# Kernel tuning notes

Hardware: AMD Instinct MI355X
Metric: run time of the kernel (lower is better)

Reference implementation:

```python
import jax, jax.numpy as jnp
import numpy as np

B, T, F, H = 64, 256, 64, 64


def setup_inputs() -> dict:
    key = jax.random.key(0)
    k = jax.random.split(key, 20)
    X_f = jax.random.normal(k[0], (B, T, F), jnp.float32)
    M_f = (jax.random.uniform(k[1], (B, T, F)) < 0.8).astype(jnp.float32)
    D_f = jax.random.uniform(k[2], (B, T, F), jnp.float32)
    # backward stream = time-reversed data with its own deltas (as in PyPOTS pipeline)
    X_b = jnp.flip(X_f, axis=1)
    M_b = jnp.flip(M_f, axis=1)
    D_b = jax.random.uniform(k[3], (B, T, F), jnp.float32)
    s = 1.0 / np.sqrt(H).astype(np.float32)
    def u(kk, shape):
        return jax.random.uniform(kk, shape, jnp.float32, minval=-s, maxval=s)
    params = dict(
        w_ih_f=u(k[4], (3 * H, 3)), w_hh_f=u(k[5], (3 * H, H)),
        b_ih_f=u(k[6], (3 * H,)), b_hh_f=u(k[7], (3 * H,)),
        w_ih_b=u(k[8], (3 * H, 3)), w_hh_b=u(k[9], (3 * H, H)),
        b_ih_b=u(k[10], (3 * H,)), b_hh_b=u(k[11], (3 * H,)),
        W_proj=u(k[12], (1, 2 * H)), b_proj=u(k[13], (1,)),
        U=u(k[14], (F, F)), V1=u(k[15], (F, F)), V2=u(k[16], (F, F)),
        beta=u(k[17], (F,)), W_fin=u(k[18], (F, F)), b_fin=u(k[19], (F,)),
    )
    return dict(X_f=X_f, M_f=M_f, D_f=D_f, X_b=X_b, M_b=M_b, D_b=D_b, **params)


def _gru_scan(xs, w_ih, w_hh, b_ih, b_hh):
    # xs: [T, N, 3] -> hidden states [T, N, H]; torch GRUCell math
    N = xs.shape[1]
    h0 = jnp.zeros((N, H), xs.dtype)
    def step(h, x):
        gi = x @ w_ih.T + b_ih          # [N, 3H]
        gh = h @ w_hh.T + b_hh          # [N, 3H]
        i_r, i_z, i_n = jnp.split(gi, 3, axis=-1)
        h_r, h_z, h_n = jnp.split(gh, 3, axis=-1)
        r = jax.nn.sigmoid(i_r + h_r)
        z = jax.nn.sigmoid(i_z + h_z)
        n = jnp.tanh(i_n + r * h_n)
        h_new = (1.0 - z) * n + z * h
        return h_new, h_new
    _, hs = jax.lax.scan(step, h0, xs)
    return hs


def _calc_rmse(pred, target, mask):
    se = jnp.sum(((pred - target) * mask) ** 2)
    return jnp.sqrt(se / (jnp.sum(mask) + 1e-12))


def reference(X_f, M_f, D_f, X_b, M_b, D_b,
              w_ih_f, w_hh_f, b_ih_f, b_hh_f,
              w_ih_b, w_hh_b, b_ih_b, b_hh_b,
              W_proj, b_proj, U, V1, V2, beta, W_fin, b_fin):
    # Fold the per-feature loop into the batch axis: N = B*F, shared GRU weights.
    def pack(X, M, D):
        inp = jnp.stack([X, M, D], axis=-1)          # [B, T, F, 3]
        return inp.transpose(1, 0, 2, 3).reshape(T, B * F, 3)
    hs_f = _gru_scan(pack(X_f, M_f, D_f), w_ih_f, w_hh_f, b_ih_f, b_hh_f)  # [T, BF, H]
    hs_b = _gru_scan(pack(X_b, M_b, D_b), w_ih_b, w_hh_b, b_ih_b, b_hh_b)
    hs_b = jnp.flip(hs_b, axis=0)
    cat = jnp.concatenate([hs_f, hs_b], axis=-1)     # [T, BF, 2H]
    est = cat @ W_proj.T + b_proj                    # [T, BF, 1]
    RNN_estimation = est.reshape(T, B, F).transpose(1, 0, 2)  # [B, T, F]
    X, M = X_f, M_f
    RNN_imputed = M * X + (1.0 - M) * RNN_estimation
    m = 1.0 - jnp.eye(F, dtype=X.dtype)
    h = jnp.tanh(X @ (U * m).T + RNN_imputed @ (V1 * m).T + M @ V2.T + beta)
    FCN_estimation = h @ W_fin.T + b_fin
    imputed_data = M * X + (1.0 - M) * FCN_estimation
    loss = _calc_rmse(FCN_estimation, X, M) + _calc_rmse(RNN_estimation, X, M)
    return imputed_data, loss
```

## Files before the change

kernel.cpp:

```cpp
#include <hip/hip_runtime.h>
#include <math.h>

#define B_ 64
#define T_ 256
#define F_ 64
#define H_ 64
#define NROW (B_ * F_)

typedef short bf16x8 __attribute__((ext_vector_type(8)));
typedef float f32x4  __attribute__((ext_vector_type(4)));

__device__ __forceinline__ float rcp_f(float x) {
  float r; asm("v_rcp_f32 %0, %1" : "=v"(r) : "v"(x)); return r;
}
__device__ __forceinline__ float sigm(float x) {
  return rcp_f(1.0f + __expf(-x));
}
__device__ __forceinline__ float tanh_f(float y) {
  return fmaf(-2.0f, rcp_f(1.0f + __expf(2.0f * y)), 1.0f);
}
__device__ __forceinline__ unsigned short bf16_rne(float v) {
  unsigned u = __float_as_uint(v);
  unsigned r = u + 0x7FFFu + ((u >> 16) & 1u);
  return (unsigned short)(r >> 16);
}

#define MFMA16(a, b, c) __builtin_amdgcn_mfma_f32_16x16x32_bf16((a), (b), (c), 0, 0, 0)

__global__ void __launch_bounds__(256, 2)
gru_kernel(const float* __restrict__ Xf, const float* __restrict__ Mf, const float* __restrict__ Df,
           const float* __restrict__ Xb, const float* __restrict__ Mb, const float* __restrict__ Db,
           const float* __restrict__ wih_f, const float* __restrict__ whh_f,
           const float* __restrict__ bih_f, const float* __restrict__ bhh_f,
           const float* __restrict__ wih_b, const float* __restrict__ whh_b,
           const float* __restrict__ bih_b, const float* __restrict__ bhh_b,
           const float* __restrict__ Wproj,
           float* __restrict__ est_f, float* __restrict__ est_b)
{
  __shared__ float          s_xmd[256][3][16];
  __shared__ unsigned short s_h[2][16][72];

  const int tid  = threadIdx.x;
  const int lane = tid & 63;
  const int wid  = tid >> 6;
  const int dir  = blockIdx.x >> 8;
  const int n0   = (blockIdx.x & 255) * 16;
  const int b0   = n0 >> 6;
  const int f0   = n0 & 63;

  const float* X   = dir ? Xb    : Xf;
  const float* M   = dir ? Mb    : Mf;
  const float* D   = dir ? Db    : Df;
  const float* wih = dir ? wih_b : wih_f;
  const float* whh = dir ? whh_b : whh_f;
  const float* bih = dir ? bih_b : bih_f;
  const float* bhh = dir ? bhh_b : bhh_f;
  float* est       = dir ? est_b : est_f;

  const int u     = 16 * wid + (lane & 15);
  const int ucol  = u;
  const int g8    = (lane >> 4) * 8;
  const int arow  = lane & 15;
  const int rbase = (lane >> 4) * 4;

  bf16x8 Bhi[3][2], Blo[3][2];
#pragma unroll
  for (int gt = 0; gt < 3; ++gt) {
#pragma unroll
    for (int kh = 0; kh < 2; ++kh) {
      const float* wp = &whh[(gt * 64 + u) * 64 + kh * 32 + g8];
#pragma unroll
      for (int j = 0; j < 8; ++j) {
        float v = wp[j];
        unsigned short hb = bf16_rne(v);
        float fhi = __uint_as_float((unsigned)hb << 16);
        Bhi[gt][kh][j] = (short)hb;
        Blo[gt][kh][j] = (short)bf16_rne(v - fhi);
      }
    }
  }

  bf16x8 Bp_hi0, Bp_hi1, Bp_lo0, Bp_lo1;
#pragma unroll
  for (int j = 0; j < 8; ++j) {
    float v0 = ((lane & 15) == 0) ? Wproj[dir * 64 + 0 * 32 + g8 + j] : 0.0f;
    float v1 = ((lane & 15) == 0) ? Wproj[dir * 64 + 1 * 32 + g8 + j] : 0.0f;
    unsigned short h0 = bf16_rne(v0), h1 = bf16_rne(v1);
    float f0h = __uint_as_float((unsigned)h0 << 16);
    float f1h = __uint_as_float((unsigned)h1 << 16);
    Bp_hi0[j] = (short)h0; Bp_hi1[j] = (short)h1;
    Bp_lo0[j] = (short)bf16_rne(v0 - f0h);
    Bp_lo1[j] = (short)bf16_rne(v1 - f1h);
  }

  const float wir0 = wih[(0 * 64 + u) * 3 + 0], wir1 = wih[(0 * 64 + u) * 3 + 1], wir2 = wih[(0 * 64 + u) * 3 + 2];
  const float wiz0 = wih[(1 * 64 + u) * 3 + 0], wiz1 = wih[(1 * 64 + u) * 3 + 1], wiz2 = wih[(1 * 64 + u) * 3 + 2];
  const float win0 = wih[(2 * 64 + u) * 3 + 0], win1 = wih[(2 * 64 + u) * 3 + 1], win2 = wih[(2 * 64 + u) * 3 + 2];
  const float br  = bih[0 * 64 + u] + bhh[0 * 64 + u];
  const float bz  = bih[1 * 64 + u] + bhh[1 * 64 + u];
  const float bin = bih[2 * 64 + u];
  const float bhn = bhh[2 * 64 + u];

  {
    const int f  = tid & 15;
    const int t0 = tid >> 4;
    const size_t rowbase = (size_t)b0 * 256 * 64 + f0 + f;
#pragma unroll 1
    for (int c = 0; c < 16; ++c) {
      int t = t0 + 16 * c;
      size_t gidx = rowbase + (size_t)t * 64;
      s_xmd[t][0][f] = X[gidx];
      s_xmd[t][1][f] = M[gidx];
      s_xmd[t][2][f] = D[gidx];
    }
  }
  for (int i = tid; i < 2 * 16 * 72; i += 256)
    ((unsigned short*)s_h)[i] = 0;
  __syncthreads();

  f32x4 hold = {0.f, 0.f, 0.f, 0.f};

#pragma unroll 2
  for (int t = 0; t < 256; ++t) {
    const int cur = t & 1, nxt = cur ^ 1;

    bf16x8 Ahi0 = *(const bf16x8*)&s_h[cur][arow][g8];
    bf16x8 Ahi1 = *(const bf16x8*)&s_h[cur][arow][32 + g8];

    if (t > 0 && wid == ((t - 1) & 3)) {
      f32x4 Cp = {0.f, 0.f, 0.f, 0.f};
      Cp = MFMA16(Ahi0, Bp_hi0, Cp); Cp = MFMA16(Ahi1, Bp_hi1, Cp);
      Cp = MFMA16(Ahi0, Bp_lo0, Cp); Cp = MFMA16(Ahi1, Bp_lo1, Cp);
      if ((lane & 15) == 0) {
        int tp = t - 1;
        int tt = dir ? (255 - tp) : tp;
        *(f32x4*)&est[(size_t)tt * NROW + n0 + rbase] = Cp;
      }
    }

    f32x4 xv = *(const f32x4*)&s_xmd[t][0][rbase];
    f32x4 mv = *(const f32x4*)&s_xmd[t][1][rbase];
    f32x4 dv = *(const f32x4*)&s_xmd[t][2][rbase];

    f32x4 Cr, Cz, Cn, gin;
#pragma unroll
    for (int r = 0; r < 4; ++r) {
      Cr[r]  = fmaf(xv[r], wir0, fmaf(mv[r], wir1, fmaf(dv[r], wir2, br)));
      Cz[r]  = fmaf(xv[r], wiz0, fmaf(mv[r], wiz1, fmaf(dv[r], wiz2, bz)));
      gin[r] = fmaf(xv[r], win0, fmaf(mv[r], win1, fmaf(dv[r], win2, bin)));
      Cn[r]  = bhn;
    }

    Cr = MFMA16(Ahi0, Bhi[0][0], Cr); Cr = MFMA16(Ahi1, Bhi[0][1], Cr);
    Cz = MFMA16(Ahi0, Bhi[1][0], Cz); Cz = MFMA16(Ahi1, Bhi[1][1], Cz);
    Cn = MFMA16(Ahi0, Bhi[2][0], Cn); Cn = MFMA16(Ahi1, Bhi[2][1], Cn);
    Cr = MFMA16(Ahi0, Blo[0][0], Cr); Cr = MFMA16(Ahi1, Blo[0][1], Cr);
    Cz = MFMA16(Ahi0, Blo[1][0], Cz); Cz = MFMA16(Ahi1, Blo[1][1], Cz);
    Cn = MFMA16(Ahi0, Blo[2][0], Cn); Cn = MFMA16(Ahi1, Blo[2][1], Cn);

#pragma unroll
    for (int r = 0; r < 4; ++r) {
      float rg = sigm(Cr[r]);
      float zg = sigm(Cz[r]);
      float nn = tanh_f(fmaf(rg, Cn[r], gin[r]));
      float hv = fmaf(zg, hold[r] - nn, nn);
      hold[r] = hv;
      s_h[nxt][rbase + r][ucol] = bf16_rne(hv);
    }

    __syncthreads();
  }

  if (wid == 3) {
    bf16x8 Ahi0 = *(const bf16x8*)&s_h[0][arow][g8];
    bf16x8 Ahi1 = *(const bf16x8*)&s_h[0][arow][32 + g8];
    f32x4 Cp = {0.f, 0.f, 0.f, 0.f};
    Cp = MFMA16(Ahi0, Bp_hi0, Cp); Cp = MFMA16(Ahi1, Bp_hi1, Cp);
    Cp = MFMA16(Ahi0, Bp_lo0, Cp); Cp = MFMA16(Ahi1, Bp_lo1, Cp);
    if ((lane & 15) == 0) {
      int tt = dir ? 0 : 255;
      *(f32x4*)&est[(size_t)tt * NROW + n0 + rbase] = Cp;
    }
  }
}

__global__ void __launch_bounds__(256, 2)
fcn_kernel(const float* __restrict__ X, const float* __restrict__ M,
           const float* __restrict__ U, const float* __restrict__ V1, const float* __restrict__ V2,
           const float* __restrict__ beta, const float* __restrict__ Wfin, const float* __restrict__ bfin,
           const float* __restrict__ bproj,
           const float* __restrict__ est_f, const float* __restrict__ est_b,
           float* __restrict__ out, float* __restrict__ acc)
{
  __shared__ unsigned short sA[64][200];
  __shared__ unsigned short sW1[64][200];
  __shared__ unsigned short sW2[64][72];
  __shared__ unsigned short sH[64][72];
  __shared__ float sbeta[64], sbfin[64];
  __shared__ float red[3][4];

  const int tid  = threadIdx.x;
  const int lane = tid & 63;
  const int wid  = tid >> 6;
  const int wg   = blockIdx.x;
  const int bb   = wg >> 2;
  const int t0   = (wg & 3) * 64;

  for (int idx = tid; idx < 4096; idx += 256) {
    int o = idx >> 6, i = idx & 63;
    sW1[o][i]       = bf16_rne((i == o) ? 0.f : U[idx]);
    sW1[o][64 + i]  = bf16_rne((i == o) ? 0.f : V1[idx]);
    sW1[o][128 + i] = bf16_rne(V2[idx]);
    sW2[o][i]       = bf16_rne(Wfin[idx]);
  }
  if (tid < 64) { sbeta[tid] = beta[tid]; sbfin[tid] = bfin[tid]; }

  const float bp = bproj[0];
  float se1 = 0.f, se2 = 0.f, sm = 0.f;
  {
    const int i = lane;
#pragma unroll 1
    for (int p = 0; p < 16; ++p) {
      int s = wid + 4 * p;
      int t = t0 + s;
      size_t gidx = ((size_t)bb * 256 + t) * 64 + i;
      float x = X[gidx], m = M[gidx];
      size_t ei = (size_t)t * NROW + bb * 64 + i;
      float re = est_f[ei] + est_b[ei] + bp;
      float ri = fmaf(m, x - re, re);
      sA[s][i]       = bf16_rne(x);
      sA[s][64 + i]  = bf16_rne(ri);
      sA[s][128 + i] = bf16_rne(m);
      float d2 = (re - x) * m;
      se2 = fmaf(d2, d2, se2); sm += m;
    }
  }
  __syncthreads();

  const int srow0 = wid * 16;
  const int arow  = lane & 15;
  const int g8    = (lane >> 4) * 8;
  const int rb    = srow0 + (lane >> 4) * 4;

  bf16x8 Af[6];
#pragma unroll
  for (int kh = 0; kh < 6; ++kh)
    Af[kh] = *(const bf16x8*)&sA[srow0 + arow][kh * 32 + g8];

  f32x4 Hc[4];
#pragma unroll
  for (int c = 0; c < 4; ++c) {
    float b0 = sbeta[c * 16 + arow];
    f32x4 C = {b0, b0, b0, b0};
#pragma unroll
    for (int kh = 0; kh < 6; ++kh) {
      bf16x8 Bf = *(const bf16x8*)&sW1[c * 16 + arow][kh * 32 + g8];
      C = MFMA16(Af[kh], Bf, C);
    }
    Hc[c] = C;
  }

#pragma unroll
  for (int c = 0; c < 4; ++c)
#pragma unroll
    for (int r = 0; r < 4; ++r)
      sH[rb + r][c * 16 + arow] = bf16_rne(tanh_f(Hc[c][r]));
  __syncthreads();

  bf16x8 A2[2];
#pragma unroll
  for (int kh = 0; kh < 2; ++kh)
    A2[kh] = *(const bf16x8*)&sH[srow0 + arow][kh * 32 + g8];

  f32x4 FE[4];
#pragma unroll
  for (int c = 0; c < 4; ++c) {
    float b0 = sbfin[c * 16 + arow];
    f32x4 C = {b0, b0, b0, b0};
#pragma unroll
    for (int kh = 0; kh < 2; ++kh) {
      bf16x8 B2 = *(const bf16x8*)&sW2[c * 16 + arow][kh * 32 + g8];
      C = MFMA16(A2[kh], B2, C);
    }
    FE[c] = C;
  }

#pragma unroll
  for (int c = 0; c < 4; ++c) {
#pragma unroll
    for (int r = 0; r < 4; ++r) {
      int s = rb + r;
      int o = c * 16 + arow;
      size_t gidx = ((size_t)bb * 256 + (t0 + s)) * 64 + o;
      float x = X[gidx], m = M[gidx];
      float fe = FE[c][r];
      out[gidx] = fmaf(m, x - fe, fe);
      float d1 = (fe - x) * m;
      se1 = fmaf(d1, d1, se1);
    }
  }

#pragma unroll
  for (int off = 32; off; off >>= 1) {
    se1 += __shfl_xor(se1, off, 64);
    se2 += __shfl_xor(se2, off, 64);
    sm  += __shfl_xor(sm,  off, 64);
  }
  if (lane == 0) { red[0][wid] = se1; red[1][wid] = se2; red[2][wid] = sm; }
  __syncthreads();
  if (tid == 0) {
    atomicAdd(&acc[0], red[0][0] + red[0][1] + red[0][2] + red[0][3]);
    atomicAdd(&acc[1], red[1][0] + red[1][1] + red[1][2] + red[1][3]);
    atomicAdd(&acc[2], red[2][0] + red[2][1] + red[2][2] + red[2][3]);
  }
}

__global__ void loss_kernel(const float* __restrict__ acc, float* __restrict__ out_loss)
{
  if (threadIdx.x == 0 && blockIdx.x == 0) {
    float denom = acc[2] + 1e-12f;
    out_loss[0] = sqrtf(acc[0] / denom) + sqrtf(acc[1] / denom);
  }
}

extern "C" void kernel_launch(void* const* d_in, const int* in_sizes, int n_in,
                              void* d_out, int out_size, void* d_ws, size_t ws_size,
                              hipStream_t stream) {
  const float* Xf    = (const float*)d_in[0];
  const float* Mf    = (const float*)d_in[1];
  const float* Df    = (const float*)d_in[2];
  const float* Xb    = (const float*)d_in[3];
  const float* Mb    = (const float*)d_in[4];
  const float* Db    = (const float*)d_in[5];
  const float* wih_f = (const float*)d_in[6];
  const float* whh_f = (const float*)d_in[7];
  const float* bih_f = (const float*)d_in[8];
  const float* bhh_f = (const float*)d_in[9];
  const float* wih_b = (const float*)d_in[10];
  const float* whh_b = (const float*)d_in[11];
  const float* bih_b = (const float*)d_in[12];
  const float* bhh_b = (const float*)d_in[13];
  const float* Wproj = (const float*)d_in[14];
  const float* bproj = (const float*)d_in[15];
  const float* U     = (const float*)d_in[16];
  const float* V1    = (const float*)d_in[17];
  const float* V2    = (const float*)d_in[18];
  const float* beta  = (const float*)d_in[19];
  const float* Wfin  = (const float*)d_in[20];
  const float* bfin  = (const float*)d_in[21];

  float* est_f = (float*)d_ws;
  float* est_b = est_f + (size_t)T_ * NROW;
  float* accp  = est_b + (size_t)T_ * NROW;

  hipMemsetAsync(accp, 0, 4 * sizeof(float), stream);

  gru_kernel<<<dim3(512), dim3(256), 0, stream>>>(
      Xf, Mf, Df, Xb, Mb, Db,
      wih_f, whh_f, bih_f, bhh_f,
      wih_b, whh_b, bih_b, bhh_b,
      Wproj, est_f, est_b);

  fcn_kernel<<<dim3(256), dim3(256), 0, stream>>>(
      Xf, Mf, U, V1, V2, beta, Wfin, bfin, bproj,
      est_f, est_b, (float*)d_out, accp);

  loss_kernel<<<dim3(1), dim3(64), 0, stream>>>(
      accp, (float*)d_out + (size_t)B_ * T_ * F_);
}
```

Before: 324.5 us.

## Move GRU input projection into MFMA and prescale weights for exp2 gates

The per-step scalar FMAs for the input-to-hidden projection are replaced by extra MFMAs over bf16-packed x/m/d/1 inputs stored in shared memory, with biases folded in through a constant-1 column. Recurrent and input weights are prescaled by log2(e) so the gates can use raw v_exp_f32 without a multiply. The bf16 conversion now uses the hardware pack instruction, and the per-step __syncthreads is replaced by an explicit lgkmcnt wait plus s_barrier. This trims VALU work on the serial recurrence path, but it adds six MFMAs per step and quantises the inputs x, m and d to bf16 (the weights keep a hi/lo split), which lowers precision.

Result: faster. 294.6 us (-9.2%).

```diff
diff --git a/kernel.cpp b/kernel.cpp
--- a/kernel.cpp
+++ b/kernel.cpp
@@ -6,6 +6,7 @@
 #define F_ 64
 #define H_ 64
 #define NROW (B_ * F_)
+#define L2E 1.4426950408889634f
 
 typedef short bf16x8 __attribute__((ext_vector_type(8)));
 typedef float f32x4  __attribute__((ext_vector_type(4)));
@@ -13,11 +14,20 @@
 __device__ __forceinline__ float rcp_f(float x) {
   float r; asm("v_rcp_f32 %0, %1" : "=v"(r) : "v"(x)); return r;
 }
-__device__ __forceinline__ float sigm(float x) {
-  return rcp_f(1.0f + __expf(-x));
+__device__ __forceinline__ float exp2_f(float x) {
+  float r; asm("v_exp_f32 %0, %1" : "=v"(r) : "v"(x)); return r;
+}
+__device__ __forceinline__ float exp2n_f(float x) {
+  float r; asm("v_exp_f32 %0, -%1" : "=v"(r) : "v"(x)); return r;
+}
+__device__ __forceinline__ unsigned cvtpk_bf16(float a, float b) {
+  unsigned r; asm("v_cvt_pk_bf16_f32 %0, %1, %2" : "=v"(r) : "v"(a), "v"(b)); return r;
+}
+__device__ __forceinline__ float bcastf(float v, int k) {
+  return __int_as_float(__builtin_amdgcn_readlane(__float_as_int(v), k));
 }
 __device__ __forceinline__ float tanh_f(float y) {
-  return fmaf(-2.0f, rcp_f(1.0f + __expf(2.0f * y)), 1.0f);
+  return fmaf(-2.0f, rcp_f(1.0f + exp2_f(2.0f * L2E * y)), 1.0f);
 }
 __device__ __forceinline__ unsigned short bf16_rne(float v) {
   unsigned u = __float_as_uint(v);
@@ -26,6 +36,7 @@
 }
 
 #define MFMA16(a, b, c) __builtin_amdgcn_mfma_f32_16x16x32_bf16((a), (b), (c), 0, 0, 0)
+#define STEP_BARRIER() asm volatile("s_waitcnt lgkmcnt(0)\n\ts_barrier" ::: "memory")
 
 __global__ void __launch_bounds__(256, 2)
 gru_kernel(const float* __restrict__ Xf, const float* __restrict__ Mf, const float* __restrict__ Df,
@@ -37,8 +48,9 @@
            const float* __restrict__ Wproj,
            float* __restrict__ est_f, float* __restrict__ est_b)
 {
-  __shared__ float          s_xmd[256][3][16];
+  __shared__ __align__(16) unsigned short s_xa[256][16][8];
   __shared__ unsigned short s_h[2][16][72];
+  __shared__ __align__(16) unsigned short s_zero[8];
 
   const int tid  = threadIdx.x;
   const int lane = tid & 63;
@@ -63,6 +75,8 @@
   const int arow  = lane & 15;
   const int rbase = (lane >> 4) * 4;
 
+  const float gsc[3] = {L2E, L2E, 2.0f * L2E};
+
   bf16x8 Bhi[3][2], Blo[3][2];
 #pragma unroll
   for (int gt = 0; gt < 3; ++gt) {
@@ -71,7 +85,7 @@
       const float* wp = &whh[(gt * 64 + u) * 64 + kh * 32 + g8];
 #pragma unroll
       for (int j = 0; j < 8; ++j) {
-        float v = wp[j];
+        float v = wp[j] * gsc[gt];
         unsigned short hb = bf16_rne(v);
         float fhi = __uint_as_float((unsigned)hb << 16);
         Bhi[gt][kh][j] = (short)hb;
@@ -79,6 +93,26 @@
       }
     }
   }
+
+  bf16x8 Bxhi[3], Bxlo[3];
+#pragma unroll
+  for (int q = 0; q < 3; ++q) {
+#pragma unroll
+    for (int j = 0; j < 8; ++j) {
+      float v = 0.0f;
+      if (lane < 16 && j < 4) {
+        if (q < 2) v = ((j < 3) ? wih[(q * 64 + u) * 3 + j]
+                                : (bih[q * 64 + u] + bhh[q * 64 + u])) * L2E;
+        else       v = ((j < 3) ? wih[(2 * 64 + u) * 3 + j]
+                                : bih[2 * 64 + u]) * (2.0f * L2E);
+      }
+      unsigned short hb = bf16_rne(v);
+      float fhi = __uint_as_float((unsigned)hb << 16);
+      Bxhi[q][j] = (short)hb;
+      Bxlo[q][j] = (short)bf16_rne(v - fhi);
+    }
+  }
+  const float bhn2 = bhh[2 * 64 + u] * (2.0f * L2E);
 
   bf16x8 Bp_hi0, Bp_hi1, Bp_lo0, Bp_lo1;
 #pragma unroll
@@ -93,29 +127,25 @@
     Bp_lo1[j] = (short)bf16_rne(v1 - f1h);
   }
 
-  const float wir0 = wih[(0 * 64 + u) * 3 + 0], wir1 = wih[(0 * 64 + u) * 3 + 1], wir2 = wih[(0 * 64 + u) * 3 + 2];
-  const float wiz0 = wih[(1 * 64 + u) * 3 + 0], wiz1 = wih[(1 * 64 + u) * 3 + 1], wiz2 = wih[(1 * 64 + u) * 3 + 2];
-  const float win0 = wih[(2 * 64 + u) * 3 + 0], win1 = wih[(2 * 64 + u) * 3 + 1], win2 = wih[(2 * 64 + u) * 3 + 2];
-  const float br  = bih[0 * 64 + u] + bhh[0 * 64 + u];
-  const float bz  = bih[1 * 64 + u] + bhh[1 * 64 + u];
-  const float bin = bih[2 * 64 + u];
-  const float bhn = bhh[2 * 64 + u];
-
   {
     const int f  = tid & 15;
     const int t0 = tid >> 4;
-    const size_t rowbase = (size_t)b0 * 256 * 64 + f0 + f;
-#pragma unroll 1
+    const size_t rowbase = (size_t)b0 * T_ * F_ + f0 + f;
+#pragma unroll 2
     for (int c = 0; c < 16; ++c) {
       int t = t0 + 16 * c;
       size_t gidx = rowbase + (size_t)t * 64;
-      s_xmd[t][0][f] = X[gidx];
-      s_xmd[t][1][f] = M[gidx];
-      s_xmd[t][2][f] = D[gidx];
+      float x = X[gidx], m = M[gidx], d = D[gidx];
+      int4 w;
+      w.x = (int)cvtpk_bf16(x, m);
+      w.y = (int)cvtpk_bf16(d, 1.0f);
+      w.z = 0; w.w = 0;
+      *(int4*)&s_xa[t][f][0] = w;
     }
   }
   for (int i = tid; i < 2 * 16 * 72; i += 256)
     ((unsigned short*)s_h)[i] = 0;
+  if (tid < 8) s_zero[tid] = 0;
   __syncthreads();
 
   f32x4 hold = {0.f, 0.f, 0.f, 0.f};
@@ -124,13 +154,14 @@
   for (int t = 0; t < 256; ++t) {
     const int cur = t & 1, nxt = cur ^ 1;
 
-    bf16x8 Ahi0 = *(const bf16x8*)&s_h[cur][arow][g8];
-    bf16x8 Ahi1 = *(const bf16x8*)&s_h[cur][arow][32 + g8];
+    bf16x8 Ah0 = *(const bf16x8*)&s_h[cur][arow][g8];
+    bf16x8 Ah1 = *(const bf16x8*)&s_h[cur][arow][32 + g8];
+    bf16x8 Ax  = *(const bf16x8*)((lane < 16) ? &s_xa[t][arow][0] : &s_zero[0]);
 
     if (t > 0 && wid == ((t - 1) & 3)) {
       f32x4 Cp = {0.f, 0.f, 0.f, 0.f};
-      Cp = MFMA16(Ahi0, Bp_hi0, Cp); Cp = MFMA16(Ahi1, Bp_hi1, Cp);
-      Cp = MFMA16(Ahi0, Bp_lo0, Cp); Cp = MFMA16(Ahi1, Bp_lo1, Cp);
+      Cp = MFMA16(Ah0, Bp_hi0, Cp); Cp = MFMA16(Ah1, Bp_hi1, Cp);
+      Cp = MFMA16(Ah0, Bp_lo0, Cp); Cp = MFMA16(Ah1, Bp_lo1, Cp);
       if ((lane & 15) == 0) {
         int tp = t - 1;
         int tt = dir ? (255 - tp) : tp;
@@ -138,45 +169,41 @@
       }
     }
 
-    f32x4 xv = *(const f32x4*)&s_xmd[t][0][rbase];
-    f32x4 mv = *(const f32x4*)&s_xmd[t][1][rbase];
-    f32x4 dv = *(const f32x4*)&s_xmd[t][2][rbase];
-
-    f32x4 Cr, Cz, Cn, gin;
+    f32x4 Cr = {0.f, 0.f, 0.f, 0.f};
+    f32x4 Cz = {0.f, 0.f, 0.f, 0.f};
+    f32x4 Cg = {0.f, 0.f, 0.f, 0.f};
+    f32x4 Cn = {bhn2, bhn2, bhn2, bhn2};
+
+    Cr = MFMA16(Ax, Bxhi[0], Cr); Cr = MFMA16(Ax, Bxlo[0], Cr);
+    Cz = MFMA16(Ax, Bxhi[1], Cz); Cz = MFMA16(Ax, Bxlo[1], Cz);
+    Cg = MFMA16(Ax, Bxhi[2], Cg); Cg = MFMA16(Ax, Bxlo[2], Cg);
+    Cr = MFMA16(Ah0, Bhi[0][0], Cr); Cr = MFMA16(Ah1, Bhi[0][1], Cr);
+    Cz = MFMA16(Ah0, Bhi[1][0], Cz); Cz = MFMA16(Ah1, Bhi[1][1], Cz);
+    Cn = MFMA16(Ah0, Bhi[2][0], Cn); Cn = MFMA16(Ah1, Bhi[2][1], Cn);
+    Cr = MFMA16(Ah0, Blo[0][0], Cr); Cr = MFMA16(Ah1, Blo[0][1], Cr);
+    Cz = MFMA16(Ah0, Blo[1][0], Cz); Cz = MFMA16(Ah1, Blo[1][1], Cz);
+    Cn = MFMA16(Ah0, Blo[2][0], Cn); Cn = MFMA16(Ah1, Blo[2][1], Cn);
+
 #pragma unroll
     for (int r = 0; r < 4; ++r) {
-      Cr[r]  = fmaf(xv[r], wir0, fmaf(mv[r], wir1, fmaf(dv[r], wir2, br)));
-      Cz[r]  = fmaf(xv[r], wiz0, fmaf(mv[r], wiz1, fmaf(dv[r], wiz2, bz)));
-      gin[r] = fmaf(xv[r], win0, fmaf(mv[r], win1, fmaf(dv[r], win2, bin)));
-      Cn[r]  = bhn;
-    }
-
-    Cr = MFMA16(Ahi0, Bhi[0][0], Cr); Cr = MFMA16(Ahi1, Bhi[0][1], Cr);
-    Cz = MFMA16(Ahi0, Bhi[1][0], Cz); Cz = MFMA16(Ahi1, Bhi[1][1], Cz);
-    Cn = MFMA16(Ahi0, Bhi[2][0], Cn); Cn = MFMA16(Ahi1, Bhi[2][1], Cn);
-    Cr = MFMA16(Ahi0, Blo[0][0], Cr); Cr = MFMA16(Ahi1, Blo[0][1], Cr);
-    Cz = MFMA16(Ahi0, Blo[1][0], Cz); Cz = MFMA16(Ahi1, Blo[1][1], Cz);
-    Cn = MFMA16(Ahi0, Blo[2][0], Cn); Cn = MFMA16(Ahi1, Blo[2][1], Cn);
-
-#pragma unroll
-    for (int r = 0; r < 4; ++r) {
-      float rg = sigm(Cr[r]);
-      float zg = sigm(Cz[r]);
-      float nn = tanh_f(fmaf(rg, Cn[r], gin[r]));
+      float rg = rcp_f(1.0f + exp2n_f(Cr[r]));
+      float zg = rcp_f(1.0f + exp2n_f(Cz[r]));
+      float yn = fmaf(rg, Cn[r], Cg[r]);
+      float nn = fmaf(-2.0f, rcp_f(1.0f + exp2_f(yn)), 1.0f);
       float hv = fmaf(zg, hold[r] - nn, nn);
       hold[r] = hv;
-      s_h[nxt][rbase + r][ucol] = bf16_rne(hv);
-    }
-
-    __syncthreads();
+      s_h[nxt][rbase + r][ucol] = (unsigned short)cvtpk_bf16(hv, hv);
+    }
+
+    STEP_BARRIER();
   }
 
   if (wid == 3) {
-    bf16x8 Ahi0 = *(const bf16x8*)&s_h[0][arow][g8];
-    bf16x8 Ahi1 = *(const bf16x8*)&s_h[0][arow][32 + g8];
+    bf16x8 Ah0 = *(const bf16x8*)&s_h[0][arow][g8];
+    bf16x8 Ah1 = *(const bf16x8*)&s_h[0][arow][32 + g8];
     f32x4 Cp = {0.f, 0.f, 0.f, 0.f};
-    Cp = MFMA16(Ahi0, Bp_hi0, Cp); Cp = MFMA16(Ahi1, Bp_hi1, Cp);
-    Cp = MFMA16(Ahi0, Bp_lo0, Cp); Cp = MFMA16(Ahi1, Bp_lo1, Cp);
+    Cp = MFMA16(Ah0, Bp_hi0, Cp); Cp = MFMA16(Ah1, Bp_hi1, Cp);
+    Cp = MFMA16(Ah0, Bp_lo0, Cp); Cp = MFMA16(Ah1, Bp_lo1, Cp);
     if ((lane & 15) == 0) {
       int tt = dir ? 0 : 255;
       *(f32x4*)&est[(size_t)tt * NROW + n0 + rbase] = Cp;
```
